# Kernel optimization log

Measured on AMD Instinct MI355X. Metric: run time of the kernel, lower is better.

The kernel has to match this reference:

```python
import jax, jax.numpy as jnp
import numpy as np

B, S, D = 2, 2048, 2048
H = 16
HD = D // H  # head_dim = 128


def setup_inputs() -> dict:
    key = jax.random.key(0)
    ks = jax.random.split(key, 5)
    scale = 1.0 / np.sqrt(D)
    x = jax.random.normal(ks[0], (B, S, D), dtype=jnp.float32)
    Wq = jax.random.normal(ks[1], (D, D), dtype=jnp.float32) * scale
    Wk = jax.random.normal(ks[2], (D, D), dtype=jnp.float32) * scale
    Wv = jax.random.normal(ks[3], (D, D), dtype=jnp.float32) * scale
    Wo = jax.random.normal(ks[4], (D, D), dtype=jnp.float32) * scale
    bo = jnp.zeros((D,), dtype=jnp.float32)
    return {"x": x, "Wq": Wq, "Wk": Wk, "Wv": Wv, "Wo": Wo, "bo": bo}


def reference(x, Wq, Wk, Wv, Wo, bo):
    b, s, _ = x.shape
    # projections (nn.Linear: y = x @ W^T, here W stored as [in, out] already)
    q = (x @ Wq).reshape(b, s, H, HD).transpose(0, 2, 1, 3)  # [B,H,S,HD]
    k = (x @ Wk).reshape(b, s, H, HD).transpose(0, 2, 1, 3)
    v = (x @ Wv).reshape(b, s, H, HD).transpose(0, 2, 1, 3)
    scores = jnp.einsum("bhqd,bhkd->bhqk", q, k)
    causal = jnp.triu(jnp.ones((s, s), dtype=bool), k=1)
    scores = jnp.where(causal[None, None], -jnp.inf, scores)
    attn = jax.nn.softmax(scores / np.sqrt(HD), axis=-1)  # dropout=0 (eval)
    out = jnp.einsum("bhqk,bhkd->bhqd", attn, v)
    out = out.transpose(0, 2, 1, 3).reshape(b, s, D)
    return out @ Wo + bo
```

## Files before the change

kernel.cpp:

```cpp
#include <hip/hip_runtime.h>

#define S_LEN 2048
#define D_MODEL 2048
#define NH 16
#define HD 128

typedef __attribute__((ext_vector_type(4))) float f32x4;
typedef __attribute__((ext_vector_type(8))) short short8;
typedef __attribute__((ext_vector_type(8))) __bf16 bf16x8;
typedef __attribute__((ext_vector_type(4))) unsigned short us4;

__device__ __forceinline__ unsigned short f2bf(float f) {
  unsigned int u = __builtin_bit_cast(unsigned int, f);
  return (unsigned short)((u + 0x7fffu + ((u >> 16) & 1u)) >> 16);
}

__device__ __forceinline__ f32x4 mfma_bf16(short8 a, short8 b, f32x4 c) {
  return __builtin_amdgcn_mfma_f32_16x16x32_bf16(
      __builtin_bit_cast(bf16x8, a), __builtin_bit_cast(bf16x8, b), c, 0, 0, 0);
}

__device__ __forceinline__ void gload16(const unsigned short* g, unsigned short* l) {
  __builtin_amdgcn_global_load_lds(
      (const __attribute__((address_space(1))) void*)g,
      (__attribute__((address_space(3))) void*)l, 16, 0, 0);
}

__global__ void cast_bf16(const float* __restrict__ src, unsigned short* __restrict__ dst, int n4) {
  int i = blockIdx.x * blockDim.x + threadIdx.x;
  if (i < n4) {
    float4 v = ((const float4*)src)[i];
    us4 o = { f2bf(v.x), f2bf(v.y), f2bf(v.z), f2bf(v.w) };
    ((us4*)dst)[i] = o;
  }
}

__global__ void transpose_cast(const float* __restrict__ W, unsigned short* __restrict__ Wt) {
  __shared__ unsigned short tile[32][33];
  int bx = blockIdx.x * 32, by = blockIdx.y * 32;
  int tx = threadIdx.x, ty = threadIdx.y;
#pragma unroll
  for (int i = 0; i < 32; i += 8)
    tile[ty + i][tx] = f2bf(W[(by + ty + i) * D_MODEL + bx + tx]);
  __syncthreads();
#pragma unroll
  for (int i = 0; i < 32; i += 8)
    Wt[(bx + ty + i) * D_MODEL + by + tx] = tile[tx][ty + i];
}

#define GEMM_KLOOP(Ag0, Ag1, Bg0, Bg1, acc, t, fu, wr, wc, lr)           \
  __shared__ unsigned short lA[3][128 * 32];                             \
  __shared__ unsigned short lB[3][128 * 32];                             \
  do {                                                                   \
    const int nt = D_MODEL >> 5;                                         \
    _Pragma("unroll") for (int i = 0; i < 2; i++) {                      \
      const int _k = i * 32;                                             \
      gload16(Ag0 + _k, lA[i] + t * 8);                                  \
      gload16(Ag1 + _k, lA[i] + 2048 + t * 8);                           \
      gload16(Bg0 + _k, lB[i] + t * 8);                                  \
      gload16(Bg1 + _k, lB[i] + 2048 + t * 8);                           \
    }                                                                    \
    int cur = 0;                                                         \
    for (int tk = 0; tk < nt; ++tk) {                                    \
      if (tk + 1 < nt) {                                                 \
        asm volatile("s_waitcnt vmcnt(4)" ::: "memory");                 \
      } else {                                                           \
        asm volatile("s_waitcnt vmcnt(0)" ::: "memory");                 \
      }                                                                  \
      __builtin_amdgcn_sched_barrier(0);                                 \
      __builtin_amdgcn_s_barrier();                                      \
      __builtin_amdgcn_sched_barrier(0);                                 \
      if (tk + 2 < nt) {                                                 \
        int nx2 = cur + 2;                                               \
        if (nx2 >= 3) nx2 -= 3;                                          \
        const int _k = (tk + 2) * 32;                                    \
        gload16(Ag0 + _k, lA[nx2] + t * 8);                              \
        gload16(Ag1 + _k, lA[nx2] + 2048 + t * 8);                       \
        gload16(Bg0 + _k, lB[nx2] + t * 8);                              \
        gload16(Bg1 + _k, lB[nx2] + 2048 + t * 8);                       \
      }                                                                  \
      const unsigned short* a = lA[cur];                                 \
      const unsigned short* b = lB[cur];                                 \
      short8 af[4], bf[4];                                               \
      _Pragma("unroll") for (int mi = 0; mi < 4; mi++)                   \
        af[mi] = *(const short8*)&a[(wr * 64 + mi * 16 + lr) * 32 + fu]; \
      _Pragma("unroll") for (int ni = 0; ni < 4; ni++)                   \
        bf[ni] = *(const short8*)&b[(wc * 64 + ni * 16 + lr) * 32 + fu]; \
      __builtin_amdgcn_s_setprio(1);                                     \
      _Pragma("unroll") for (int mi = 0; mi < 4; mi++)                   \
        _Pragma("unroll") for (int ni = 0; ni < 4; ni++)                 \
          acc[mi][ni] = mfma_bf16(af[mi], bf[ni], acc[mi][ni]);          \
      __builtin_amdgcn_s_setprio(0);                                     \
      cur = (cur == 2) ? 0 : cur + 1;                                    \
    }                                                                    \
  } while (0)

__global__ __launch_bounds__(256, 2) void gemm_qkv(
    const unsigned short* __restrict__ A, const unsigned short* __restrict__ Bt,
    unsigned short* __restrict__ qb, unsigned short* __restrict__ kb,
    unsigned short* __restrict__ vtb) {
  const int t = threadIdx.x;
  const int l = t & 63, w = t >> 6;
  const int wr = w >> 1, wc = w & 1;
  const int lr = l & 15, lk = l >> 4;
  const int n0 = blockIdx.x * 128, m0 = blockIdx.y * 128;

  const int arow = t >> 2;
  const int au = ((t & 3) ^ ((arow >> 1) & 3)) * 8;
  const unsigned short* Ag0 = A + (size_t)(m0 + arow) * D_MODEL + au;
  const unsigned short* Ag1 = Ag0 + 64 * D_MODEL;
  const unsigned short* Bg0 = Bt + (size_t)(n0 + arow) * D_MODEL + au;
  const unsigned short* Bg1 = Bg0 + 64 * D_MODEL;
  const int fu = (lk ^ ((lr >> 1) & 3)) * 8;

  f32x4 acc[4][4] = {};
  GEMM_KLOOP(Ag0, Ag1, Bg0, Bg1, acc, t, fu, wr, wc, lr);

  if (n0 < 4096) {
    unsigned short* C = (n0 < 2048) ? qb : kb;
    const int nbase = n0 & 2047;
#pragma unroll
    for (int mi = 0; mi < 4; mi++) {
      int r0 = m0 + wr * 64 + mi * 16 + lk * 4;
#pragma unroll
      for (int ni = 0; ni < 4; ni++) {
        int c2 = nbase + wc * 64 + ni * 16 + lr;
#pragma unroll
        for (int r = 0; r < 4; r++)
          C[(size_t)(r0 + r) * D_MODEL + c2] = f2bf(acc[mi][ni][r]);
      }
    }
  } else {
    const int nb = n0 - 4096;
#pragma unroll
    for (int mi = 0; mi < 4; mi++) {
      int s = m0 + wr * 64 + mi * 16 + lk * 4;
#pragma unroll
      for (int ni = 0; ni < 4; ni++) {
        int n = nb + wc * 64 + ni * 16 + lr;
        int h = n >> 7, d = n & (HD - 1);
        us4 pk = { f2bf(acc[mi][ni][0]), f2bf(acc[mi][ni][1]),
                   f2bf(acc[mi][ni][2]), f2bf(acc[mi][ni][3]) };
        *(us4*)&vtb[((size_t)(h * HD + d)) * S_LEN + s] = pk;
      }
    }
  }
}

__global__ __launch_bounds__(256, 2) void gemm_out(
    const unsigned short* __restrict__ ctx0, const unsigned short* __restrict__ ctx1,
    const unsigned short* __restrict__ Bt, const float* __restrict__ bias,
    float* __restrict__ out) {
  const int t = threadIdx.x;
  const int l = t & 63, w = t >> 6;
  const int wr = w >> 1, wc = w & 1;
  const int lr = l & 15, lk = l >> 4;
  const int n0 = blockIdx.x * 128, m0 = blockIdx.y * 128;

  const unsigned short* Ablk = (m0 < 2048)
      ? ctx0 + (size_t)m0 * D_MODEL
      : ctx1 + (size_t)(m0 - 2048) * D_MODEL;

  const int arow = t >> 2;
  const int au = ((t & 3) ^ ((arow >> 1) & 3)) * 8;
  const unsigned short* Ag0 = Ablk + (size_t)arow * D_MODEL + au;
  const unsigned short* Ag1 = Ag0 + 64 * D_MODEL;
  const unsigned short* Bg0 = Bt + (size_t)(n0 + arow) * D_MODEL + au;
  const unsigned short* Bg1 = Bg0 + 64 * D_MODEL;
  const int fu = (lk ^ ((lr >> 1) & 3)) * 8;

  f32x4 acc[4][4] = {};
  GEMM_KLOOP(Ag0, Ag1, Bg0, Bg1, acc, t, fu, wr, wc, lr);

#pragma unroll
  for (int mi = 0; mi < 4; mi++) {
    int r0 = m0 + wr * 64 + mi * 16 + lk * 4;
#pragma unroll
    for (int ni = 0; ni < 4; ni++) {
      int c2 = n0 + wc * 64 + ni * 16 + lr;
      float bv = bias[c2];
#pragma unroll
      for (int r = 0; r < 4; r++)
        out[(size_t)(r0 + r) * D_MODEL + c2] = acc[mi][ni][r] + bv;
    }
  }
}

__global__ __launch_bounds__(256, 2) void attn_kernel(
    const unsigned short* __restrict__ Q, const unsigned short* __restrict__ K,
    const unsigned short* __restrict__ Vt, unsigned short* __restrict__ ctx) {
  __shared__ unsigned short lds[28672];
  unsigned short* lK0 = lds;
  unsigned short* lK1 = lds + 8192;
  unsigned short* lV  = lds + 16384;
  unsigned short* lP  = lds + 24576;

  const int id = blockIdx.x;
  const int h = id & 15;
  const int qtl = id >> 4;
  const int qt = (qtl < 16) ? (2 * qtl) : (63 - 2 * qtl);

  const int t = threadIdx.x, l = t & 63, w = t >> 6;
  const int lr = l & 15, lk = l >> 4;

  const unsigned short* qsrc = Q + (size_t)(qt * 64 + w * 16 + lr) * D_MODEL + h * HD;
  short8 Qf[4];
#pragma unroll
  for (int kk = 0; kk < 4; kk++)
    Qf[kk] = *(const short8*)&qsrc[kk * 32 + lk * 8];

  const unsigned short* ksrc = K + h * HD;
  const unsigned short* vsrc = Vt + (size_t)h * HD * S_LEN;

  const int krow = t >> 4;
  const int kcs  = t & 15;
  const int vrow = t >> 3;
  const int vcs  = t & 7;

  f32x4 O[8] = {};
  float mrow[4] = {-1e30f, -1e30f, -1e30f, -1e30f};
  float lrow[4] = {0.f, 0.f, 0.f, 0.f};

  const int nkv = qt + 1;
  const float scale = 0.08838834764831845f;

#pragma unroll
  for (int i = 0; i < 4; i++) {
    int row = i * 16 + krow;
    gload16(ksrc + (size_t)row * D_MODEL + ((kcs ^ (row & 7)) * 8),
            lK0 + row * 128 + kcs * 8);
  }

  for (int tk = 0; tk < nkv; tk++) {
    const int kv0 = tk * 64;
    unsigned short* lKc = (tk & 1) ? lK1 : lK0;
    unsigned short* lKn = (tk & 1) ? lK0 : lK1;
    const bool more = (tk + 1 < nkv);

#pragma unroll
    for (int i = 0; i < 4; i++) {
      int row = i * 32 + vrow;
      gload16(vsrc + (size_t)row * S_LEN + kv0 + ((vcs ^ (row & 7)) * 8),
              lV + row * 64 + vcs * 8);
    }
    if (more) {
#pragma unroll
      for (int i = 0; i < 4; i++) {
        int row = i * 16 + krow;
        gload16(ksrc + (size_t)(kv0 + 64 + row) * D_MODEL + ((kcs ^ (row & 7)) * 8),
                lKn + row * 128 + kcs * 8);
      }
      asm volatile("s_waitcnt vmcnt(8)" ::: "memory");
    } else {
      asm volatile("s_waitcnt vmcnt(4)" ::: "memory");
    }
    __builtin_amdgcn_sched_barrier(0);
    __builtin_amdgcn_s_barrier();
    __builtin_amdgcn_sched_barrier(0);

    f32x4 sc[4] = {};
    __builtin_amdgcn_s_setprio(1);
#pragma unroll
    for (int kk = 0; kk < 4; kk++) {
      short8 Kf[4];
#pragma unroll
      for (int ni = 0; ni < 4; ni++)
        Kf[ni] = *(const short8*)&lKc[(ni * 16 + lr) * 128 + (((kk * 4 + lk) ^ (lr & 7)) * 8)];
#pragma unroll
      for (int ni = 0; ni < 4; ni++)
        sc[ni] = mfma_bf16(Qf[kk], Kf[ni], sc[ni]);
    }
    __builtin_amdgcn_s_setprio(0);

    const bool diag = (tk == qt);
    const int row0 = qt * 64 + w * 16 + lk * 4;
#pragma unroll
    for (int ni = 0; ni < 4; ni++) {
      const int col = kv0 + ni * 16 + lr;
#pragma unroll
      for (int r = 0; r < 4; r++) {
        float v = sc[ni][r] * scale;
        if (diag && col > row0 + r) v = -1e30f;
        sc[ni][r] = v;
      }
    }
#pragma unroll
    for (int r = 0; r < 4; r++) {
      float rm = fmaxf(fmaxf(sc[0][r], sc[1][r]), fmaxf(sc[2][r], sc[3][r]));
      rm = fmaxf(rm, __shfl_xor(rm, 1));
      rm = fmaxf(rm, __shfl_xor(rm, 2));
      rm = fmaxf(rm, __shfl_xor(rm, 4));
      rm = fmaxf(rm, __shfl_xor(rm, 8));
      const float mo = mrow[r];
      const float mn = fmaxf(mo, rm);
      const float al = __expf(mo - mn);
      float rs = 0.f;
#pragma unroll
      for (int ni = 0; ni < 4; ni++) {
        const float p = __expf(sc[ni][r] - mn);
        sc[ni][r] = p;
        rs += p;
      }
      rs += __shfl_xor(rs, 1);
      rs += __shfl_xor(rs, 2);
      rs += __shfl_xor(rs, 4);
      rs += __shfl_xor(rs, 8);
      mrow[r] = mn;
      lrow[r] = lrow[r] * al + rs;
#pragma unroll
      for (int di = 0; di < 8; di++) O[di][r] *= al;
    }

    unsigned short* lPw = lP + w * 1024;
#pragma unroll
    for (int ni = 0; ni < 4; ni++)
#pragma unroll
      for (int r = 0; r < 4; r++) {
        int prow = lk * 4 + r;
        int pu = (ni * 2 + (lr >> 3)) ^ (prow & 7);
        lPw[prow * 64 + pu * 8 + (lr & 7)] = f2bf(sc[ni][r]);
      }

    if (more) {
      asm volatile("s_waitcnt vmcnt(4)" ::: "memory");
    } else {
      asm volatile("s_waitcnt vmcnt(0)" ::: "memory");
    }
    __builtin_amdgcn_sched_barrier(0);
    __builtin_amdgcn_s_barrier();
    __builtin_amdgcn_sched_barrier(0);

    __builtin_amdgcn_s_setprio(1);
#pragma unroll
    for (int kk = 0; kk < 2; kk++) {
      short8 Pf = *(const short8*)&lPw[lr * 64 + (((kk * 4 + lk) ^ (lr & 7)) * 8)];
#pragma unroll
      for (int di = 0; di < 8; di++) {
        short8 Vf = *(const short8*)&lV[(di * 16 + lr) * 64 + (((kk * 4 + lk) ^ (lr & 7)) * 8)];
        O[di] = mfma_bf16(Pf, Vf, O[di]);
      }
    }
    __builtin_amdgcn_s_setprio(0);

    __builtin_amdgcn_s_barrier();
    __builtin_amdgcn_sched_barrier(0);
  }

#pragma unroll
  for (int di = 0; di < 8; di++) {
#pragma unroll
    for (int r = 0; r < 4; r++) {
      float v = O[di][r] / lrow[r];
      ctx[(size_t)(qt * 64 + w * 16 + lk * 4 + r) * D_MODEL + h * HD + di * 16 + lr] = f2bf(v);
    }
  }
}

extern "C" void kernel_launch(void* const* d_in, const int* in_sizes, int n_in,
                              void* d_out, int out_size, void* d_ws, size_t ws_size,
                              hipStream_t stream) {
  const float* x  = (const float*)d_in[0];
  const float* Wq = (const float*)d_in[1];
  const float* Wk = (const float*)d_in[2];
  const float* Wv = (const float*)d_in[3];
  const float* Wo = (const float*)d_in[4];
  const float* bo = (const float*)d_in[5];
  float* out = (float*)d_out;

  unsigned short* ws = (unsigned short*)d_ws;
  unsigned short* S0 = ws;
  unsigned short* S1 = ws + 1 * 4194304;
  unsigned short* S2 = ws + 2 * 4194304;
  unsigned short* S3 = ws + 3 * 4194304;
  unsigned short* S4 = ws + 4 * 4194304;
  unsigned short* wqkvt = (unsigned short*)d_out;

  dim3 tb(32, 8), tg(64, 64);

  transpose_cast<<<tg, tb, 0, stream>>>(Wq, wqkvt);
  transpose_cast<<<tg, tb, 0, stream>>>(Wk, wqkvt + 4194304);
  transpose_cast<<<tg, tb, 0, stream>>>(Wv, wqkvt + 2 * 4194304);

  for (int b = 0; b < 2; b++) {
    const float* xbatch = x + (size_t)b * S_LEN * D_MODEL;
    unsigned short* ctx = (b == 0) ? S4 : S0;

    cast_bf16<<<4096, 256, 0, stream>>>(xbatch, S0, 1048576);
    gemm_qkv<<<dim3(48, 16), 256, 0, stream>>>(S0, wqkvt, S1, S2, S3);
    attn_kernel<<<dim3(512), 256, 0, stream>>>(S1, S2, S3, ctx);
  }

  transpose_cast<<<tg, tb, 0, stream>>>(Wo, S1);
  gemm_out<<<dim3(16, 32), 256, 0, stream>>>(S4, S0, S1, bo, out);
}
```

Measured before the change: 343.3 us.

## Double-buffer K and V tiles, transpose score MFMA, fold softmax scale into Q

The attention kernel now double-buffers both K and V in LDS. Each iteration needs one barrier instead of three, and the next tile's loads are issued right after that barrier. The QK^T MFMA operands are swapped so each lane holds one query row, which replaces the per-row 16-lane shuffle reductions with a single per-lane reduction plus two shuffles. The softmax scale and log2(e) are folded into Q at load time so exp2 can be used directly, and P is written to LDS as packed 4-element stores. LDS use grows from 56 KB to 72 KB per block, and pre-scaling Q in bf16 adds a small rounding change.

```diff
diff --git a/kernel.cpp b/kernel.cpp
--- a/kernel.cpp
+++ b/kernel.cpp
@@ -189,11 +189,7 @@
 __global__ __launch_bounds__(256, 2) void attn_kernel(
     const unsigned short* __restrict__ Q, const unsigned short* __restrict__ K,
     const unsigned short* __restrict__ Vt, unsigned short* __restrict__ ctx) {
-  __shared__ unsigned short lds[28672];
-  unsigned short* lK0 = lds;
-  unsigned short* lK1 = lds + 8192;
-  unsigned short* lV  = lds + 16384;
-  unsigned short* lP  = lds + 24576;
+  __shared__ unsigned short lds[36864];
 
   const int id = blockIdx.x;
   const int h = id & 15;
@@ -203,61 +199,62 @@
   const int t = threadIdx.x, l = t & 63, w = t >> 6;
   const int lr = l & 15, lk = l >> 4;
 
+  const float qscale = 0.08838834764831845f * 1.44269504088896340f;
   const unsigned short* qsrc = Q + (size_t)(qt * 64 + w * 16 + lr) * D_MODEL + h * HD;
   short8 Qf[4];
 #pragma unroll
-  for (int kk = 0; kk < 4; kk++)
-    Qf[kk] = *(const short8*)&qsrc[kk * 32 + lk * 8];
+  for (int kk = 0; kk < 4; kk++) {
+    short8 qv = *(const short8*)&qsrc[kk * 32 + lk * 8];
+#pragma unroll
+    for (int e = 0; e < 8; e++) {
+      unsigned int u = ((unsigned int)(unsigned short)qv[e]) << 16;
+      float f = __builtin_bit_cast(float, u) * qscale;
+      qv[e] = (short)f2bf(f);
+    }
+    Qf[kk] = qv;
+  }
 
   const unsigned short* ksrc = K + h * HD;
   const unsigned short* vsrc = Vt + (size_t)h * HD * S_LEN;
-
-  const int krow = t >> 4;
-  const int kcs  = t & 15;
-  const int vrow = t >> 3;
-  const int vcs  = t & 7;
+  const int krow = t >> 4, kcs = t & 15;
+  const int vrow = t >> 3, vcs = t & 7;
+
+#define STAGE_KV(par, kv0base)                                                    \
+  do {                                                                            \
+    unsigned short* lKb = lds + (par) * 8192;                                     \
+    unsigned short* lVb = lds + 16384 + (par) * 8192;                             \
+    _Pragma("unroll") for (int i = 0; i < 4; i++) {                               \
+      int row = i * 16 + krow;                                                    \
+      gload16(ksrc + (size_t)((kv0base) + row) * D_MODEL + ((kcs ^ (row & 7)) * 8), \
+              lKb + row * 128 + kcs * 8);                                         \
+    }                                                                             \
+    _Pragma("unroll") for (int i = 0; i < 4; i++) {                               \
+      int row = i * 32 + vrow;                                                    \
+      gload16(vsrc + (size_t)row * S_LEN + (kv0base) + ((vcs ^ (row & 7)) * 8),   \
+              lVb + row * 64 + vcs * 8);                                          \
+    }                                                                             \
+  } while (0)
 
   f32x4 O[8] = {};
-  float mrow[4] = {-1e30f, -1e30f, -1e30f, -1e30f};
-  float lrow[4] = {0.f, 0.f, 0.f, 0.f};
-
+  float m_s = -1e30f, l_s = 0.f;
   const int nkv = qt + 1;
-  const float scale = 0.08838834764831845f;
-
-#pragma unroll
-  for (int i = 0; i < 4; i++) {
-    int row = i * 16 + krow;
-    gload16(ksrc + (size_t)row * D_MODEL + ((kcs ^ (row & 7)) * 8),
-            lK0 + row * 128 + kcs * 8);
-  }
+  unsigned short* lPw = lds + 32768 + w * 1024;
+
+  STAGE_KV(0, 0);
 
   for (int tk = 0; tk < nkv; tk++) {
     const int kv0 = tk * 64;
-    unsigned short* lKc = (tk & 1) ? lK1 : lK0;
-    unsigned short* lKn = (tk & 1) ? lK0 : lK1;
-    const bool more = (tk + 1 < nkv);
-
-#pragma unroll
-    for (int i = 0; i < 4; i++) {
-      int row = i * 32 + vrow;
-      gload16(vsrc + (size_t)row * S_LEN + kv0 + ((vcs ^ (row & 7)) * 8),
-              lV + row * 64 + vcs * 8);
-    }
-    if (more) {
-#pragma unroll
-      for (int i = 0; i < 4; i++) {
-        int row = i * 16 + krow;
-        gload16(ksrc + (size_t)(kv0 + 64 + row) * D_MODEL + ((kcs ^ (row & 7)) * 8),
-                lKn + row * 128 + kcs * 8);
-      }
-      asm volatile("s_waitcnt vmcnt(8)" ::: "memory");
-    } else {
-      asm volatile("s_waitcnt vmcnt(4)" ::: "memory");
-    }
+    const int par = tk & 1;
+    const unsigned short* lKc = lds + par * 8192;
+    const unsigned short* lVc = lds + 16384 + par * 8192;
+
+    asm volatile("s_waitcnt vmcnt(0)" ::: "memory");
     __builtin_amdgcn_sched_barrier(0);
     __builtin_amdgcn_s_barrier();
     __builtin_amdgcn_sched_barrier(0);
 
+    if (tk + 1 < nkv) STAGE_KV(par ^ 1, kv0 + 64);
+
     f32x4 sc[4] = {};
     __builtin_amdgcn_s_setprio(1);
 #pragma unroll
@@ -268,67 +265,58 @@
         Kf[ni] = *(const short8*)&lKc[(ni * 16 + lr) * 128 + (((kk * 4 + lk) ^ (lr & 7)) * 8)];
 #pragma unroll
       for (int ni = 0; ni < 4; ni++)
-        sc[ni] = mfma_bf16(Qf[kk], Kf[ni], sc[ni]);
+        sc[ni] = mfma_bf16(Kf[ni], Qf[kk], sc[ni]);
     }
     __builtin_amdgcn_s_setprio(0);
 
-    const bool diag = (tk == qt);
-    const int row0 = qt * 64 + w * 16 + lk * 4;
-#pragma unroll
-    for (int ni = 0; ni < 4; ni++) {
-      const int col = kv0 + ni * 16 + lr;
+    const int row0g = qt * 64 + w * 16 + lr;
+    if (tk == qt) {
+#pragma unroll
+      for (int ni = 0; ni < 4; ni++) {
+        const int colb = kv0 + ni * 16 + lk * 4;
+#pragma unroll
+        for (int r = 0; r < 4; r++)
+          if (colb + r > row0g) sc[ni][r] = -1e30f;
+      }
+    }
+
+    f32x4 mx4;
+#pragma unroll
+    for (int r = 0; r < 4; r++)
+      mx4[r] = fmaxf(fmaxf(sc[0][r], sc[1][r]), fmaxf(sc[2][r], sc[3][r]));
+    float pm = fmaxf(fmaxf(mx4[0], mx4[1]), fmaxf(mx4[2], mx4[3]));
+    pm = fmaxf(pm, __shfl_xor(pm, 16));
+    pm = fmaxf(pm, __shfl_xor(pm, 32));
+    const float mn = fmaxf(m_s, pm);
+    const float al = __builtin_amdgcn_exp2f(m_s - mn);
+    float rs = 0.f;
+#pragma unroll
+    for (int ni = 0; ni < 4; ni++)
 #pragma unroll
       for (int r = 0; r < 4; r++) {
-        float v = sc[ni][r] * scale;
-        if (diag && col > row0 + r) v = -1e30f;
-        sc[ni][r] = v;
-      }
-    }
-#pragma unroll
-    for (int r = 0; r < 4; r++) {
-      float rm = fmaxf(fmaxf(sc[0][r], sc[1][r]), fmaxf(sc[2][r], sc[3][r]));
-      rm = fmaxf(rm, __shfl_xor(rm, 1));
-      rm = fmaxf(rm, __shfl_xor(rm, 2));
-      rm = fmaxf(rm, __shfl_xor(rm, 4));
-      rm = fmaxf(rm, __shfl_xor(rm, 8));
-      const float mo = mrow[r];
-      const float mn = fmaxf(mo, rm);
-      const float al = __expf(mo - mn);
-      float rs = 0.f;
-#pragma unroll
-      for (int ni = 0; ni < 4; ni++) {
-        const float p = __expf(sc[ni][r] - mn);
+        float p = __builtin_amdgcn_exp2f(sc[ni][r] - mn);
         sc[ni][r] = p;
         rs += p;
       }
-      rs += __shfl_xor(rs, 1);
-      rs += __shfl_xor(rs, 2);
-      rs += __shfl_xor(rs, 4);
-      rs += __shfl_xor(rs, 8);
-      mrow[r] = mn;
-      lrow[r] = lrow[r] * al + rs;
-#pragma unroll
-      for (int di = 0; di < 8; di++) O[di][r] *= al;
-    }
-
-    unsigned short* lPw = lP + w * 1024;
-#pragma unroll
-    for (int ni = 0; ni < 4; ni++)
-#pragma unroll
-      for (int r = 0; r < 4; r++) {
-        int prow = lk * 4 + r;
-        int pu = (ni * 2 + (lr >> 3)) ^ (prow & 7);
-        lPw[prow * 64 + pu * 8 + (lr & 7)] = f2bf(sc[ni][r]);
-      }
-
-    if (more) {
-      asm volatile("s_waitcnt vmcnt(4)" ::: "memory");
-    } else {
-      asm volatile("s_waitcnt vmcnt(0)" ::: "memory");
-    }
-    __builtin_amdgcn_sched_barrier(0);
-    __builtin_amdgcn_s_barrier();
-    __builtin_amdgcn_sched_barrier(0);
+    rs += __shfl_xor(rs, 16);
+    rs += __shfl_xor(rs, 32);
+    m_s = mn;
+    l_s = l_s * al + rs;
+
+    float al4[4];
+#pragma unroll
+    for (int r = 0; r < 4; r++) al4[r] = __shfl(al, lk * 4 + r);
+#pragma unroll
+    for (int di = 0; di < 8; di++)
+#pragma unroll
+      for (int r = 0; r < 4; r++) O[di][r] *= al4[r];
+
+#pragma unroll
+    for (int ni = 0; ni < 4; ni++) {
+      us4 pk = { f2bf(sc[ni][0]), f2bf(sc[ni][1]), f2bf(sc[ni][2]), f2bf(sc[ni][3]) };
+      int u16 = (ni * 2 + (lk >> 1)) ^ (lr & 7);
+      *(us4*)&lPw[lr * 64 + u16 * 8 + (lk & 1) * 4] = pk;
+    }
 
     __builtin_amdgcn_s_setprio(1);
 #pragma unroll
@@ -336,24 +324,24 @@
       short8 Pf = *(const short8*)&lPw[lr * 64 + (((kk * 4 + lk) ^ (lr & 7)) * 8)];
 #pragma unroll
       for (int di = 0; di < 8; di++) {
-        short8 Vf = *(const short8*)&lV[(di * 16 + lr) * 64 + (((kk * 4 + lk) ^ (lr & 7)) * 8)];
+        short8 Vf = *(const short8*)&lVc[(di * 16 + lr) * 64 + (((kk * 4 + lk) ^ (lr & 7)) * 8)];
         O[di] = mfma_bf16(Pf, Vf, O[di]);
       }
     }
     __builtin_amdgcn_s_setprio(0);
-
-    __builtin_amdgcn_s_barrier();
-    __builtin_amdgcn_sched_barrier(0);
-  }
-
-#pragma unroll
-  for (int di = 0; di < 8; di++) {
+  }
+#undef STAGE_KV
+
+  float lr4[4];
+#pragma unroll
+  for (int r = 0; r < 4; r++) lr4[r] = __shfl(l_s, lk * 4 + r);
+#pragma unroll
+  for (int di = 0; di < 8; di++)
 #pragma unroll
     for (int r = 0; r < 4; r++) {
-      float v = O[di][r] / lrow[r];
+      float v = O[di][r] / lr4[r];
       ctx[(size_t)(qt * 64 + w * 16 + lk * 4 + r) * D_MODEL + h * HD + di * 16 + lr] = f2bf(v);
     }
-  }
 }
 
 extern "C" void kernel_launch(void* const* d_in, const int* in_sizes, int n_in,
```

Result: faster. 300.9 us (-12.3%).
